# Kernel tuning notes

Hardware: AMD Instinct MI355X
Metric: run time of the kernel (lower is better)

Reference implementation:

```python
import jax, jax.numpy as jnp
import numpy as np

S, M, V, E, H = 128, 256, 32000, 1024, 512
PAD_ID = V - 1  # pad_id=-1 normalized to vocab-1


def setup_inputs() -> dict:
    key = jax.random.key(0)
    ks = jax.random.split(key, 9)
    F_lens = jax.random.randint(ks[0], (M,), 1, S + 1)
    tok = jax.random.randint(ks[1], (S, M), 1, PAD_ID)  # avoid 0 and PAD for valid tokens
    valid = jnp.arange(S)[:, None] < F_lens[None, :]
    F = jnp.where(valid, tok, PAD_ID)
    sc = 1.0 / np.sqrt(H)
    emb = jax.random.normal(ks[2], (V, E), jnp.float32) * 0.02
    emb = emb.at[PAD_ID].set(0.0)
    # PyTorch LSTM layout: gates [i, f, g, o]; bias_ih + bias_hh folded into one b.
    Wih0 = jax.random.uniform(ks[3], (2, 4 * H, E), jnp.float32, -sc, sc)
    Whh0 = jax.random.uniform(ks[4], (2, 4 * H, H), jnp.float32, -sc, sc)
    b0 = jax.random.uniform(ks[5], (2, 4 * H), jnp.float32, -sc, sc)
    Wih1 = jax.random.uniform(ks[6], (2, 4 * H, 2 * H), jnp.float32, -sc, sc)
    Whh1 = jax.random.uniform(ks[7], (2, 4 * H, H), jnp.float32, -sc, sc)
    b1 = jax.random.uniform(ks[8], (2, 4 * H), jnp.float32, -sc, sc)
    return dict(F=F, F_lens=F_lens, emb=emb, Wih0=Wih0, Whh0=Whh0, b0=b0,
                Wih1=Wih1, Whh1=Whh1, b1=b1)


def _run_lstm(x, mask, Wih, Whh, b):
    # x: [S, M, D], mask: [S, M] bool (update state only where valid, as packed seq does)
    m_ = x.shape[1]
    h_dim = Whh.shape[1]

    def step(carry, inp):
        h, c = carry
        xt, mt = inp
        g = xt @ Wih.T + h @ Whh.T + b
        i, f, gg, o = jnp.split(g, 4, axis=-1)
        c2 = jax.nn.sigmoid(f) * c + jax.nn.sigmoid(i) * jnp.tanh(gg)
        h2 = jax.nn.sigmoid(o) * jnp.tanh(c2)
        mt = mt[:, None]
        h2 = jnp.where(mt, h2, h)
        c2 = jnp.where(mt, c2, c)
        return (h2, c2), h2

    init = (jnp.zeros((m_, h_dim), x.dtype), jnp.zeros((m_, h_dim), x.dtype))
    _, hs = jax.lax.scan(step, init, (x, mask))
    return hs


def _bilstm_layer(x, mask, idx, Wih, Whh, b):
    # forward direction
    hf = _run_lstm(x, mask, Wih[0], Whh[0], b[0])
    # backward direction: per-sequence reverse within valid length (packed semantics)
    xr = jnp.take_along_axis(x, idx[:, :, None], axis=0)
    hb = _run_lstm(xr, mask, Wih[1], Whh[1], b[1])
    hb = jnp.take_along_axis(hb, idx[:, :, None], axis=0)  # idx is an involution on valid t
    return jnp.concatenate([hf, hb], axis=-1)


def reference(F, F_lens, emb, Wih0, Whh0, b0, Wih1, Whh1, b1):
    s_ = F.shape[0]
    t = jnp.arange(s_)[:, None]
    valid = t < F_lens[None, :]                      # [S, M]
    idx = jnp.where(valid, F_lens[None, :] - 1 - t, t)
    # embedding with padding_idx zeroing (matches nn.Embedding padding_idx + explicit loop)
    x = jnp.where((F != PAD_ID)[:, :, None], emb[F], 0.0)
    h1 = _bilstm_layer(x, valid, idx, Wih0, Whh0, b0)
    h2 = _bilstm_layer(h1, valid, idx, Wih1, Whh1, b1)
    # pad_packed_sequence(padding_value=h_pad=0) + final F==0 masking loop, fused
    keep = valid & (F != 0)
    return jnp.where(keep[:, :, None], h2, 0.0)
```

## Files before the change

kernel.cpp:

```cpp
#include <hip/hip_runtime.h>
#include <hip/hip_bf16.h>

#define S_LEN 128
#define M_B   256
#define E_DIM 1024
#define H_DIM 512
#define G4    2048
#define N_ROWS (S_LEN*M_B)
#define KD    1024

typedef __bf16 bf16_t;
typedef __bf16 bf16x8 __attribute__((ext_vector_type(8)));
typedef float  f32x4  __attribute__((ext_vector_type(4)));
typedef int    i32x4  __attribute__((ext_vector_type(4)));

#define AS1(p) ((const __attribute__((address_space(1))) void*)(p))
#define AS3(p) ((__attribute__((address_space(3))) void*)(p))

__device__ __forceinline__ float sigm(float x)     { return 1.f / (1.f + __expf(-x)); }
__device__ __forceinline__ float tanhfast(float x) { return 2.f / (1.f + __expf(-2.f * x)) - 1.f; }

__device__ __forceinline__ void store_h_dev(bf16_t* p, bf16_t v) {
    unsigned int w = (unsigned int)__builtin_bit_cast(unsigned short, v);
    asm volatile("global_store_short %0, %1, off sc0 sc1" :: "v"(p), "v"(w) : "memory");
}
__device__ __forceinline__ bf16x8 load_h_dev(const bf16_t* p) {
    i32x4 r;
    asm volatile("global_load_dwordx4 %0, %1, off sc0 sc1" : "=v"(r) : "v"(p) : "memory");
    return __builtin_bit_cast(bf16x8, r);
}
__device__ __forceinline__ float load_f32_async(const float* p) {
    float r;
    asm volatile("global_load_dword %0, %1, off" : "=v"(r) : "v"(p) : "memory");
    return r;
}

__global__ __launch_bounds__(256)
void permute_all_kernel(const float* __restrict__ Wih0, const float* __restrict__ Whh0,
                        const float* __restrict__ b0,
                        const float* __restrict__ Wih1, const float* __restrict__ Whh1,
                        const float* __restrict__ b1,
                        bf16_t* __restrict__ Wih0p, bf16_t* __restrict__ Whh0p,
                        bf16_t* __restrict__ Wih1p, bf16_t* __restrict__ Whh1p,
                        float* __restrict__ b0p, float* __restrict__ b1p)
{
    int bid = blockIdx.x;
    int lay = bid >> 12;
    int d   = (bid >> 11) & 1;
    int jp  = bid & 2047;
    int q = jp >> 6, r = jp & 63;
    int gate = r >> 4, u16 = r & 15;
    int j = gate * H_DIM + q * 16 + u16;

    const float* Wih = lay ? Wih1 : Wih0;
    const float* Whh = lay ? Whh1 : Whh0;
    const float* b   = lay ? b1 : b0;
    bf16_t* Wihp = lay ? Wih1p : Wih0p;
    bf16_t* Whhp = lay ? Whh1p : Whh0p;
    float*  bp   = lay ? b1p : b0p;

    const float* s_ih = Wih + ((size_t)d * G4 + j) * E_DIM;
    bf16_t*      d_ih = Wihp + ((size_t)d * G4 + jp) * E_DIM;
    for (int e = threadIdx.x; e < E_DIM; e += 256) d_ih[e] = (bf16_t)s_ih[e];

    const float* s_hh = Whh + ((size_t)d * G4 + j) * H_DIM;
    bf16_t*      d_hh = Whhp + ((size_t)d * G4 + jp) * H_DIM;
    for (int k = threadIdx.x; k < H_DIM; k += 256) d_hh[k] = (bf16_t)s_hh[k];

    if (threadIdx.x == 0) bp[d * G4 + jp] = b[d * G4 + j];
}

__global__ __launch_bounds__(256)
void embed_kernel(const int* __restrict__ F, const float* __restrict__ emb,
                  const int* __restrict__ F_lens,
                  bf16_t* __restrict__ X, int* __restrict__ srcrow)
{
    int n   = blockIdx.x;
    int tok = F[n];
    const float4* src = (const float4*)(emb + (size_t)tok * E_DIM);
    bf16_t*       dst = X + (size_t)n * E_DIM;
    for (int i = threadIdx.x; i < E_DIM / 4; i += 256) {
        float4 v = src[i];
        dst[i * 4 + 0] = (bf16_t)v.x;
        dst[i * 4 + 1] = (bf16_t)v.y;
        dst[i * 4 + 2] = (bf16_t)v.z;
        dst[i * 4 + 3] = (bf16_t)v.w;
    }
    if (threadIdx.x == 0) {
        int t = n >> 8, m = n & 255;
        int L = F_lens[m];
        int st = (t < L) ? (L - 1 - t) : t;
        srcrow[n] = st * M_B + m;
    }
}

#define BM 128
#define BN 128
#define BKG 64

__global__ __launch_bounds__(256)
void gemm_pre_kernel(const bf16_t* __restrict__ A,
                     const bf16_t* __restrict__ Wp,
                     const float* __restrict__ bp,
                     const int* __restrict__ srcrow,
                     float* __restrict__ PREc,
                     int rowbase, int TCR)
{
    const int nwg = gridDim.x;
    const int qx  = nwg >> 3;
    const int orig = blockIdx.x;
    const int wg   = (orig & 7) * qx + (orig >> 3);
    const int MT   = TCR / BM;
    const int n_t  = wg & 15;
    const int m_t  = (wg >> 4) % MT;
    const int d    = wg / (16 * MT);

    const int n0   = n_t * BN;
    const int mloc = m_t * BM;
    const int tid  = threadIdx.x;
    const int lane = tid & 63, wave = tid >> 6;
    const int wm = wave >> 1, wn = wave & 1;
    const int fr = lane & 15, fq = lane >> 4;

    __shared__ __attribute__((aligned(16))) bf16_t At[BM * BKG];
    __shared__ __attribute__((aligned(16))) bf16_t Bt[BN * BKG];

    const int rA = tid >> 3;
    const int co = (((tid & 7) ^ (rA & 7)) << 3);
    size_t srowA[4];
    const bf16_t* Bp[4];
#pragma unroll
    for (int it = 0; it < 4; ++it) {
        int nn = rowbase + mloc + rA + it * 32;
        srowA[it] = (d == 1) ? (size_t)srcrow[nn] : (size_t)nn;
        Bp[it] = Wp + ((size_t)d * G4 + n0 + rA + it * 32) * KD + co;
    }

    f32x4 acc[4][4];
#pragma unroll
    for (int i = 0; i < 4; ++i)
#pragma unroll
        for (int j = 0; j < 4; ++j) { f32x4 z = {0.f, 0.f, 0.f, 0.f}; acc[i][j] = z; }

    for (int kt = 0; kt < KD; kt += BKG) {
#pragma unroll
        for (int it = 0; it < 4; ++it)
            __builtin_amdgcn_global_load_lds(AS1(A + srowA[it] * KD + kt + co),
                                             AS3(&At[(it * 256 + wave * 64) * 8]), 16, 0, 0);
#pragma unroll
        for (int it = 0; it < 4; ++it)
            __builtin_amdgcn_global_load_lds(AS1(Bp[it] + kt),
                                             AS3(&Bt[(it * 256 + wave * 64) * 8]), 16, 0, 0);
        __syncthreads();

        bf16x8 af[2][4], bff[2][4];
#pragma unroll
        for (int ks = 0; ks < 2; ++ks) {
#pragma unroll
            for (int i = 0; i < 4; ++i) {
                int ra = wm * 64 + i * 16 + fr;
                int ca = (ks * 4 + fq) ^ (ra & 7);
                af[ks][i] = *(const bf16x8*)&At[ra * BKG + ca * 8];
                int rb = wn * 64 + i * 16 + fr;
                int cbk = (ks * 4 + fq) ^ (rb & 7);
                bff[ks][i] = *(const bf16x8*)&Bt[rb * BKG + cbk * 8];
            }
        }
#pragma unroll
        for (int ks = 0; ks < 2; ++ks)
#pragma unroll
            for (int i = 0; i < 4; ++i)
#pragma unroll
                for (int j = 0; j < 4; ++j)
                    acc[i][j] = __builtin_amdgcn_mfma_f32_16x16x32_bf16(af[ks][i], bff[ks][j], acc[i][j], 0, 0, 0);
        __syncthreads();
    }

    const int cb = n0 + wn * 64 + fr;
#pragma unroll
    for (int mi = 0; mi < 4; ++mi) {
#pragma unroll
        for (int rr = 0; rr < 4; ++rr) {
            int r = mloc + wm * 64 + mi * 16 + fq * 4 + rr;
            float* prow = PREc + ((size_t)d * TCR + r) * G4;
#pragma unroll
            for (int ni = 0; ni < 4; ++ni) {
                int col = cb + ni * 16;
                prow[col] = acc[mi][ni][rr] + bp[d * G4 + col];
            }
        }
    }
}

__global__ __launch_bounds__(256)
void lstm_chunk_kernel(const bf16_t* __restrict__ Whhp,
                       const float* __restrict__ PREc,
                       const int* __restrict__ F_lens,
                       float* __restrict__ cfb,
                       bf16_t* __restrict__ hbA,
                       bf16_t* __restrict__ hbB,
                       bf16_t* __restrict__ H1,
                       float* __restrict__ OUT,
                       unsigned int* __restrict__ ctr,
                       int t0, int TC, int TCR, int mode, int s_base)
{
    const int d  = blockIdx.z;
    const int bx = blockIdx.x;
    const int m0 = blockIdx.y * 64;
    const int tid = threadIdx.x;
    const int lane = tid & 63, wave = tid >> 6;
    const int fr = lane & 15, fq = lane >> 4;
    const int gslot = ((blockIdx.y << 1) | d) * 16;

    __shared__ __attribute__((aligned(16))) bf16_t Bt[64 * 512];

    const bf16_t* Bg = Whhp + ((size_t)d * G4 + bx * 64) * H_DIM;
#pragma unroll
    for (int it = 0; it < 16; ++it) {
        int c   = it * 256 + tid;
        int row = c >> 6, ck = c & 63;
        int cks = ck ^ (row & 7);
        __builtin_amdgcn_global_load_lds(AS1(Bg + (size_t)row * H_DIM + cks * 8),
                                         AS3(&Bt[(it * 256 + wave * 64) * 8]), 16, 0, 0);
    }

    const int mrow  = m0 + wave * 16 + fr;
    const int u     = bx * 16 + fr;
    const int cbcol = bx * 64 + fr;
    int mm[4], LL[4], sidx[4];
    float c_own[4], h_own[4];
    const float* pbase[4];
#pragma unroll
    for (int rr = 0; rr < 4; ++rr) {
        mm[rr]   = m0 + wave * 16 + fq * 4 + rr;
        LL[rr]   = F_lens[mm[rr]];
        sidx[rr] = (d * M_B + mm[rr]) * H_DIM + u;
        c_own[rr]= cfb[sidx[rr]];
        pbase[rr]= PREc + ((size_t)d * TCR + mm[rr]) * G4 + cbcol;
    }
    {
        const bf16_t* hin0 = (t0 & 1) ? hbB : hbA;
#pragma unroll
        for (int rr = 0; rr < 4; ++rr) h_own[rr] = (float)hin0[sidx[rr]];
    }

    float pv[4][4];
#pragma unroll
    for (int rr = 0; rr < 4; ++rr) {
#pragma unroll
        for (int g = 0; g < 4; ++g)
            pv[rr][g] = load_f32_async(pbase[rr] + g * 16);
    }

    __syncthreads();

    for (int tt = 0; tt < TC; ++tt) {
        const int t = t0 + tt;
        const bf16_t* hin  = (t & 1) ? hbB : hbA;
        bf16_t*       hout = (t & 1) ? hbA : hbB;

        const bf16_t* Arow = hin + ((size_t)d * M_B + mrow) * H_DIM + fq * 8;
        bf16x8 af[16];
#pragma unroll
        for (int ks = 0; ks < 16; ++ks)
            af[ks] = load_h_dev(Arow + ks * 32);
        asm volatile("s_waitcnt vmcnt(0)" ::: "memory");
        __builtin_amdgcn_sched_barrier(0);

        f32x4 acc[4];
#pragma unroll
        for (int j = 0; j < 4; ++j) { f32x4 z = {0.f, 0.f, 0.f, 0.f}; acc[j] = z; }

#pragma unroll
        for (int ks = 0; ks < 16; ++ks) {
#pragma unroll
            for (int j = 0; j < 4; ++j) {
                int rb = j * 16 + fr;
                int ck = (ks * 4 + fq) ^ (rb & 7);
                bf16x8 bf = *(const bf16x8*)&Bt[rb * 512 + ck * 8];
                acc[j] = __builtin_amdgcn_mfma_f32_16x16x32_bf16(af[ks], bf, acc[j], 0, 0, 0);
            }
        }

#pragma unroll
        for (int rr = 0; rr < 4; ++rr) {
            bool mt = (t < LL[rr]);
            float gi = acc[0][rr] + pv[rr][0];
            float gf = acc[1][rr] + pv[rr][1];
            float gg = acc[2][rr] + pv[rr][2];
            float go = acc[3][rr] + pv[rr][3];
            float c2 = sigm(gf) * c_own[rr] + sigm(gi) * tanhfast(gg);
            float h2 = sigm(go) * tanhfast(c2);
            if (!mt) { c2 = c_own[rr]; h2 = h_own[rr]; }
            c_own[rr] = c2;
            h_own[rr] = h2;
            store_h_dev(&hout[sidx[rr]], (bf16_t)h2);
        }
        asm volatile("s_waitcnt vmcnt(0)" ::: "memory");
        __syncthreads();
        if (tid == 0)
            __hip_atomic_fetch_add(&ctr[gslot], 1u, __ATOMIC_RELAXED, __HIP_MEMORY_SCOPE_AGENT);

#pragma unroll
        for (int rr = 0; rr < 4; ++rr) {
            bool mt = (t < LL[rr]);
            int trow = (d == 0 || !mt) ? t : (LL[rr] - 1 - t);
            size_t orow = (size_t)trow * M_B + mm[rr];
            if (mode == 0) H1[orow * 1024 + d * H_DIM + u] = (bf16_t)h_own[rr];
            else           OUT[orow * 1024 + d * H_DIM + u] = mt ? h_own[rr] : 0.f;
        }
        float pvn[4][4];
        if (tt + 1 < TC) {
#pragma unroll
            for (int rr = 0; rr < 4; ++rr) {
                const float* prow = pbase[rr] + (size_t)(tt + 1) * ((size_t)M_B * G4);
#pragma unroll
                for (int g = 0; g < 4; ++g)
                    pvn[rr][g] = load_f32_async(prow + g * 16);
            }
        }

        if (tid == 0) {
            unsigned int tgt = (unsigned int)(s_base + tt + 1) * 32u;
            while (__hip_atomic_load(&ctr[gslot], __ATOMIC_RELAXED, __HIP_MEMORY_SCOPE_AGENT) < tgt)
                __builtin_amdgcn_s_sleep(2);
        }
        __syncthreads();

        if (tt + 1 < TC) {
#pragma unroll
            for (int rr = 0; rr < 4; ++rr)
#pragma unroll
                for (int g = 0; g < 4; ++g)
                    pv[rr][g] = pvn[rr][g];
        }
    }

#pragma unroll
    for (int rr = 0; rr < 4; ++rr) cfb[sidx[rr]] = c_own[rr];
}

extern "C" void kernel_launch(void* const* d_in, const int* in_sizes, int n_in,
                              void* d_out, int out_size, void* d_ws, size_t ws_size,
                              hipStream_t stream)
{
    const int*   F      = (const int*)d_in[0];
    const int*   F_lens = (const int*)d_in[1];
    const float* emb    = (const float*)d_in[2];
    const float* Wih0   = (const float*)d_in[3];
    const float* Whh0   = (const float*)d_in[4];
    const float* b0     = (const float*)d_in[5];
    const float* Wih1   = (const float*)d_in[6];
    const float* Whh1   = (const float*)d_in[7];
    const float* b1     = (const float*)d_in[8];
    float* OUT = (float*)d_out;

    char* p = (char*)d_ws;
    auto alloc = [&](size_t bytes) { char* q = p; p += (bytes + 255) & ~(size_t)255; return (void*)q; };
    bf16_t* X0    = (bf16_t*)alloc((size_t)N_ROWS * E_DIM * 2);
    bf16_t* H1    = (bf16_t*)alloc((size_t)N_ROWS * 1024 * 2);
    bf16_t* Wih0p = (bf16_t*)alloc((size_t)2 * G4 * E_DIM * 2);
    bf16_t* Whh0p = (bf16_t*)alloc((size_t)2 * G4 * H_DIM * 2);
    bf16_t* Wih1p = (bf16_t*)alloc((size_t)2 * G4 * E_DIM * 2);
    bf16_t* Whh1p = (bf16_t*)alloc((size_t)2 * G4 * H_DIM * 2);
    float*  b0p   = (float*)alloc((size_t)2 * G4 * 4);
    float*  b1p   = (float*)alloc((size_t)2 * G4 * 4);
    int*    srcrow= (int*)alloc((size_t)N_ROWS * 4);
    bf16_t* hbA   = (bf16_t*)alloc((size_t)2 * M_B * H_DIM * 2);
    bf16_t* hbB   = (bf16_t*)alloc((size_t)2 * M_B * H_DIM * 2);
    float*  cfb   = (float*)alloc((size_t)2 * M_B * H_DIM * 4);
    unsigned int* ctr = (unsigned int*)alloc(512);
    size_t base_used = (size_t)(p - (char*)d_ws);

    int TC = 0;
    const int tcs[6] = {32, 16, 8, 4, 2, 1};
    for (int i = 0; i < 6; ++i) {
        size_t need = base_used + (size_t)2 * tcs[i] * M_B * G4 * 4;
        if (need <= ws_size) { TC = tcs[i]; break; }
    }
    if (TC == 0) return;
    float* PREc = (float*)p;
    const int TCR = TC * M_B;

    hipMemsetAsync(ctr, 0, 512, stream);
    permute_all_kernel<<<dim3(2 * 2 * G4), 256, 0, stream>>>(
        Wih0, Whh0, b0, Wih1, Whh1, b1, Wih0p, Whh0p, Wih1p, Whh1p, b0p, b1p);
    embed_kernel<<<dim3(N_ROWS), 256, 0, stream>>>(F, emb, F_lens, X0, srcrow);

    for (int layer = 0; layer < 2; ++layer) {
        const bf16_t* Xin  = layer ? H1 : X0;
        const bf16_t* Wihp = layer ? Wih1p : Wih0p;
        const bf16_t* Whhp = layer ? Whh1p : Whh0p;
        const float*  bp   = layer ? b1p : b0p;

        hipMemsetAsync(hbA, 0, (size_t)2 * M_B * H_DIM * 2, stream);
        hipMemsetAsync(cfb, 0, (size_t)2 * M_B * H_DIM * 4, stream);

        for (int c = 0; c < S_LEN / TC; ++c) {
            gemm_pre_kernel<<<dim3(2 * (TCR / BM) * 16), 256, 0, stream>>>(
                Xin, Wihp, bp, srcrow, PREc, c * TCR, TCR);

            lstm_chunk_kernel<<<dim3(32, 4, 2), dim3(256), 0, stream>>>(
                Whhp, PREc, F_lens, cfb, hbA, hbB, H1, OUT, ctr,
                c * TC, TC, TCR, layer, layer * S_LEN + c * TC);
        }
    }
}
```

Before: 2.418 ms.

## Fuse input projection into persistent LSTM layer kernel, drop precomputed gate buffer

Measured after the change: 5.757 ms. 138% more time.

```diff
diff --git a/kernel.cpp b/kernel.cpp
--- a/kernel.cpp
+++ b/kernel.cpp
@@ -7,7 +7,6 @@
 #define H_DIM 512
 #define G4    2048
 #define N_ROWS (S_LEN*M_B)
-#define KD    1024
 
 typedef __bf16 bf16_t;
 typedef __bf16 bf16x8 __attribute__((ext_vector_type(8)));
@@ -28,11 +27,6 @@
     i32x4 r;
     asm volatile("global_load_dwordx4 %0, %1, off sc0 sc1" : "=v"(r) : "v"(p) : "memory");
     return __builtin_bit_cast(bf16x8, r);
-}
-__device__ __forceinline__ float load_f32_async(const float* p) {
-    float r;
-    asm volatile("global_load_dword %0, %1, off" : "=v"(r) : "v"(p) : "memory");
-    return r;
 }
 
 __global__ __launch_bounds__(256)
@@ -72,8 +66,7 @@
 
 __global__ __launch_bounds__(256)
 void embed_kernel(const int* __restrict__ F, const float* __restrict__ emb,
-                  const int* __restrict__ F_lens,
-                  bf16_t* __restrict__ X, int* __restrict__ srcrow)
+                  bf16_t* __restrict__ X)
 {
     int n   = blockIdx.x;
     int tok = F[n];
@@ -86,124 +79,22 @@
         dst[i * 4 + 2] = (bf16_t)v.z;
         dst[i * 4 + 3] = (bf16_t)v.w;
     }
-    if (threadIdx.x == 0) {
-        int t = n >> 8, m = n & 255;
-        int L = F_lens[m];
-        int st = (t < L) ? (L - 1 - t) : t;
-        srcrow[n] = st * M_B + m;
-    }
-}
-
-#define BM 128
-#define BN 128
-#define BKG 64
+}
 
 __global__ __launch_bounds__(256)
-void gemm_pre_kernel(const bf16_t* __restrict__ A,
-                     const bf16_t* __restrict__ Wp,
-                     const float* __restrict__ bp,
-                     const int* __restrict__ srcrow,
-                     float* __restrict__ PREc,
-                     int rowbase, int TCR)
-{
-    const int nwg = gridDim.x;
-    const int qx  = nwg >> 3;
-    const int orig = blockIdx.x;
-    const int wg   = (orig & 7) * qx + (orig >> 3);
-    const int MT   = TCR / BM;
-    const int n_t  = wg & 15;
-    const int m_t  = (wg >> 4) % MT;
-    const int d    = wg / (16 * MT);
-
-    const int n0   = n_t * BN;
-    const int mloc = m_t * BM;
-    const int tid  = threadIdx.x;
-    const int lane = tid & 63, wave = tid >> 6;
-    const int wm = wave >> 1, wn = wave & 1;
-    const int fr = lane & 15, fq = lane >> 4;
-
-    __shared__ __attribute__((aligned(16))) bf16_t At[BM * BKG];
-    __shared__ __attribute__((aligned(16))) bf16_t Bt[BN * BKG];
-
-    const int rA = tid >> 3;
-    const int co = (((tid & 7) ^ (rA & 7)) << 3);
-    size_t srowA[4];
-    const bf16_t* Bp[4];
-#pragma unroll
-    for (int it = 0; it < 4; ++it) {
-        int nn = rowbase + mloc + rA + it * 32;
-        srowA[it] = (d == 1) ? (size_t)srcrow[nn] : (size_t)nn;
-        Bp[it] = Wp + ((size_t)d * G4 + n0 + rA + it * 32) * KD + co;
-    }
-
-    f32x4 acc[4][4];
-#pragma unroll
-    for (int i = 0; i < 4; ++i)
-#pragma unroll
-        for (int j = 0; j < 4; ++j) { f32x4 z = {0.f, 0.f, 0.f, 0.f}; acc[i][j] = z; }
-
-    for (int kt = 0; kt < KD; kt += BKG) {
-#pragma unroll
-        for (int it = 0; it < 4; ++it)
-            __builtin_amdgcn_global_load_lds(AS1(A + srowA[it] * KD + kt + co),
-                                             AS3(&At[(it * 256 + wave * 64) * 8]), 16, 0, 0);
-#pragma unroll
-        for (int it = 0; it < 4; ++it)
-            __builtin_amdgcn_global_load_lds(AS1(Bp[it] + kt),
-                                             AS3(&Bt[(it * 256 + wave * 64) * 8]), 16, 0, 0);
-        __syncthreads();
-
-        bf16x8 af[2][4], bff[2][4];
-#pragma unroll
-        for (int ks = 0; ks < 2; ++ks) {
-#pragma unroll
-            for (int i = 0; i < 4; ++i) {
-                int ra = wm * 64 + i * 16 + fr;
-                int ca = (ks * 4 + fq) ^ (ra & 7);
-                af[ks][i] = *(const bf16x8*)&At[ra * BKG + ca * 8];
-                int rb = wn * 64 + i * 16 + fr;
-                int cbk = (ks * 4 + fq) ^ (rb & 7);
-                bff[ks][i] = *(const bf16x8*)&Bt[rb * BKG + cbk * 8];
-            }
-        }
-#pragma unroll
-        for (int ks = 0; ks < 2; ++ks)
-#pragma unroll
-            for (int i = 0; i < 4; ++i)
-#pragma unroll
-                for (int j = 0; j < 4; ++j)
-                    acc[i][j] = __builtin_amdgcn_mfma_f32_16x16x32_bf16(af[ks][i], bff[ks][j], acc[i][j], 0, 0, 0);
-        __syncthreads();
-    }
-
-    const int cb = n0 + wn * 64 + fr;
-#pragma unroll
-    for (int mi = 0; mi < 4; ++mi) {
-#pragma unroll
-        for (int rr = 0; rr < 4; ++rr) {
-            int r = mloc + wm * 64 + mi * 16 + fq * 4 + rr;
-            float* prow = PREc + ((size_t)d * TCR + r) * G4;
-#pragma unroll
-            for (int ni = 0; ni < 4; ++ni) {
-                int col = cb + ni * 16;
-                prow[col] = acc[mi][ni][rr] + bp[d * G4 + col];
-            }
-        }
-    }
-}
-
-__global__ __launch_bounds__(256)
-void lstm_chunk_kernel(const bf16_t* __restrict__ Whhp,
-                       const float* __restrict__ PREc,
+void lstm_layer_kernel(const bf16_t* __restrict__ Whhp,
+                       const bf16_t* __restrict__ Wihp,
+                       const float* __restrict__ bp,
+                       const bf16_t* __restrict__ Xin,
                        const int* __restrict__ F_lens,
-                       float* __restrict__ cfb,
                        bf16_t* __restrict__ hbA,
                        bf16_t* __restrict__ hbB,
                        bf16_t* __restrict__ H1,
                        float* __restrict__ OUT,
                        unsigned int* __restrict__ ctr,
-                       int t0, int TC, int TCR, int mode, int s_base)
-{
+                       int mode, int s_base)
+{
+    const int TC = S_LEN;
     const int d  = blockIdx.z;
     const int bx = blockIdx.x;
     const int m0 = blockIdx.y * 64;
@@ -227,68 +118,83 @@
     const int mrow  = m0 + wave * 16 + fr;
     const int u     = bx * 16 + fr;
     const int cbcol = bx * 64 + fr;
+    const int Lm    = F_lens[mrow];
     int mm[4], LL[4], sidx[4];
     float c_own[4], h_own[4];
-    const float* pbase[4];
+    float bias[4];
+    const bf16_t* wihb[4];
+#pragma unroll
+    for (int j = 0; j < 4; ++j) {
+        bias[j] = bp[d * G4 + cbcol + j * 16];
+        wihb[j] = Wihp + ((size_t)d * G4 + bx * 64 + j * 16 + fr) * E_DIM + fq * 8;
+    }
 #pragma unroll
     for (int rr = 0; rr < 4; ++rr) {
         mm[rr]   = m0 + wave * 16 + fq * 4 + rr;
         LL[rr]   = F_lens[mm[rr]];
         sidx[rr] = (d * M_B + mm[rr]) * H_DIM + u;
-        c_own[rr]= cfb[sidx[rr]];
-        pbase[rr]= PREc + ((size_t)d * TCR + mm[rr]) * G4 + cbcol;
-    }
+        c_own[rr] = 0.f;
+        h_own[rr] = 0.f;
+    }
+
+    f32x4 acc[4];
+#pragma unroll
+    for (int j = 0; j < 4; ++j) { f32x4 z = {0.f, 0.f, 0.f, 0.f}; acc[j] = z; }
     {
-        const bf16_t* hin0 = (t0 & 1) ? hbB : hbA;
-#pragma unroll
-        for (int rr = 0; rr < 4; ++rr) h_own[rr] = (float)hin0[sidx[rr]];
-    }
-
-    float pv[4][4];
-#pragma unroll
-    for (int rr = 0; rr < 4; ++rr) {
-#pragma unroll
-        for (int g = 0; g < 4; ++g)
-            pv[rr][g] = load_f32_async(pbase[rr] + g * 16);
+        const int trx = (d == 0) ? 0 : (Lm - 1);
+        const bf16_t* Xrow = Xin + ((size_t)trx * M_B + mrow) * E_DIM + fq * 8;
+#pragma unroll
+        for (int half = 0; half < 2; ++half) {
+            bf16x8 ax[16];
+#pragma unroll
+            for (int ks = 0; ks < 16; ++ks)
+                ax[ks] = *(const bf16x8*)(Xrow + half * 512 + ks * 32);
+#pragma unroll
+            for (int ks = 0; ks < 16; ++ks) {
+#pragma unroll
+                for (int j = 0; j < 4; ++j) {
+                    bf16x8 bw = *(const bf16x8*)(wihb[j] + half * 512 + ks * 32);
+                    acc[j] = __builtin_amdgcn_mfma_f32_16x16x32_bf16(ax[ks], bw, acc[j], 0, 0, 0);
+                }
+            }
+        }
     }
 
     __syncthreads();
 
     for (int tt = 0; tt < TC; ++tt) {
-        const int t = t0 + tt;
+        const int t = tt;
         const bf16_t* hin  = (t & 1) ? hbB : hbA;
         bf16_t*       hout = (t & 1) ? hbA : hbB;
 
-        const bf16_t* Arow = hin + ((size_t)d * M_B + mrow) * H_DIM + fq * 8;
-        bf16x8 af[16];
-#pragma unroll
-        for (int ks = 0; ks < 16; ++ks)
-            af[ks] = load_h_dev(Arow + ks * 32);
-        asm volatile("s_waitcnt vmcnt(0)" ::: "memory");
-        __builtin_amdgcn_sched_barrier(0);
-
-        f32x4 acc[4];
-#pragma unroll
-        for (int j = 0; j < 4; ++j) { f32x4 z = {0.f, 0.f, 0.f, 0.f}; acc[j] = z; }
-
-#pragma unroll
-        for (int ks = 0; ks < 16; ++ks) {
-#pragma unroll
-            for (int j = 0; j < 4; ++j) {
-                int rb = j * 16 + fr;
-                int ck = (ks * 4 + fq) ^ (rb & 7);
-                bf16x8 bf = *(const bf16x8*)&Bt[rb * 512 + ck * 8];
-                acc[j] = __builtin_amdgcn_mfma_f32_16x16x32_bf16(af[ks], bf, acc[j], 0, 0, 0);
+        if (t > 0) {
+            const bf16_t* Arow = hin + ((size_t)d * M_B + mrow) * H_DIM + fq * 8;
+            bf16x8 af[16];
+#pragma unroll
+            for (int ks = 0; ks < 16; ++ks)
+                af[ks] = load_h_dev(Arow + ks * 32);
+            asm volatile("s_waitcnt vmcnt(0)" ::: "memory");
+            __builtin_amdgcn_sched_barrier(0);
+
+#pragma unroll
+            for (int ks = 0; ks < 16; ++ks) {
+#pragma unroll
+                for (int j = 0; j < 4; ++j) {
+                    int rb = j * 16 + fr;
+                    int ck = (ks * 4 + fq) ^ (rb & 7);
+                    bf16x8 bf = *(const bf16x8*)&Bt[rb * 512 + ck * 8];
+                    acc[j] = __builtin_amdgcn_mfma_f32_16x16x32_bf16(af[ks], bf, acc[j], 0, 0, 0);
+                }
             }
         }
 
 #pragma unroll
         for (int rr = 0; rr < 4; ++rr) {
             bool mt = (t < LL[rr]);
-            float gi = acc[0][rr] + pv[rr][0];
-            float gf = acc[1][rr] + pv[rr][1];
-            float gg = acc[2][rr] + pv[rr][2];
-            float go = acc[3][rr] + pv[rr][3];
+            float gi = acc[0][rr] + bias[0];
+            float gf = acc[1][rr] + bias[1];
+            float gg = acc[2][rr] + bias[2];
+            float go = acc[3][rr] + bias[3];
             float c2 = sigm(gf) * c_own[rr] + sigm(gi) * tanhfast(gg);
             float h2 = sigm(go) * tanhfast(c2);
             if (!mt) { c2 = c_own[rr]; h2 = h_own[rr]; }
@@ -309,14 +215,27 @@
             if (mode == 0) H1[orow * 1024 + d * H_DIM + u] = (bf16_t)h_own[rr];
             else           OUT[orow * 1024 + d * H_DIM + u] = mt ? h_own[rr] : 0.f;
         }
-        float pvn[4][4];
+
+#pragma unroll
+        for (int j = 0; j < 4; ++j) { f32x4 z = {0.f, 0.f, 0.f, 0.f}; acc[j] = z; }
         if (tt + 1 < TC) {
-#pragma unroll
-            for (int rr = 0; rr < 4; ++rr) {
-                const float* prow = pbase[rr] + (size_t)(tt + 1) * ((size_t)M_B * G4);
-#pragma unroll
-                for (int g = 0; g < 4; ++g)
-                    pvn[rr][g] = load_f32_async(prow + g * 16);
+            const int tn  = t + 1;
+            const int trx = (d == 0 || tn >= Lm) ? tn : (Lm - 1 - tn);
+            const bf16_t* Xrow = Xin + ((size_t)trx * M_B + mrow) * E_DIM + fq * 8;
+#pragma unroll
+            for (int half = 0; half < 2; ++half) {
+                bf16x8 ax[16];
+#pragma unroll
+                for (int ks = 0; ks < 16; ++ks)
+                    ax[ks] = *(const bf16x8*)(Xrow + half * 512 + ks * 32);
+#pragma unroll
+                for (int ks = 0; ks < 16; ++ks) {
+#pragma unroll
+                    for (int j = 0; j < 4; ++j) {
+                        bf16x8 bw = *(const bf16x8*)(wihb[j] + half * 512 + ks * 32);
+                        acc[j] = __builtin_amdgcn_mfma_f32_16x16x32_bf16(ax[ks], bw, acc[j], 0, 0, 0);
+                    }
+                }
             }
         }
 
@@ -326,18 +245,7 @@
                 __builtin_amdgcn_s_sleep(2);
         }
         __syncthreads();
-
-        if (tt + 1 < TC) {
-#pragma unroll
-            for (int rr = 0; rr < 4; ++rr)
-#pragma unroll
-                for (int g = 0; g < 4; ++g)
-                    pv[rr][g] = pvn[rr][g];
-        }
-    }
-
-#pragma unroll
-    for (int rr = 0; rr < 4; ++rr) cfb[sidx[rr]] = c_own[rr];
+    }
 }
 
 extern "C" void kernel_launch(void* const* d_in, const int* in_sizes, int n_in,
@@ -365,44 +273,18 @@
     bf16_t* Whh1p = (bf16_t*)alloc((size_t)2 * G4 * H_DIM * 2);
     float*  b0p   = (float*)alloc((size_t)2 * G4 * 4);
     float*  b1p   = (float*)alloc((size_t)2 * G4 * 4);
-    int*    srcrow= (int*)alloc((size_t)N_ROWS * 4);
     bf16_t* hbA   = (bf16_t*)alloc((size_t)2 * M_B * H_DIM * 2);
     bf16_t* hbB   = (bf16_t*)alloc((size_t)2 * M_B * H_DIM * 2);
-    float*  cfb   = (float*)alloc((size_t)2 * M_B * H_DIM * 4);
     unsigned int* ctr = (unsigned int*)alloc(512);
-    size_t base_used = (size_t)(p - (char*)d_ws);
-
-    int TC = 0;
-    const int tcs[6] = {32, 16, 8, 4, 2, 1};
-    for (int i = 0; i < 6; ++i) {
-        size_t need = base_used + (size_t)2 * tcs[i] * M_B * G4 * 4;
-        if (need <= ws_size) { TC = tcs[i]; break; }
-    }
-    if (TC == 0) return;
-    float* PREc = (float*)p;
-    const int TCR = TC * M_B;
+    if (ws_size < (size_t)(p - (char*)d_ws)) return;
 
     hipMemsetAsync(ctr, 0, 512, stream);
     permute_all_kernel<<<dim3(2 * 2 * G4), 256, 0, stream>>>(
         Wih0, Whh0, b0, Wih1, Whh1, b1, Wih0p, Whh0p, Wih1p, Whh1p, b0p, b1p);
-    embed_kernel<<<dim3(N_ROWS), 256, 0, stream>>>(F, emb, F_lens, X0, srcrow);
-
-    for (int layer = 0; layer < 2; ++layer) {
-        const bf16_t* Xin  = layer ? H1 : X0;
-        const bf16_t* Wihp = layer ? Wih1p : Wih0p;
-        const bf16_t* Whhp = layer ? Whh1p : Whh0p;
-        const float*  bp   = layer ? b1p : b0p;
-
-        hipMemsetAsync(hbA, 0, (size_t)2 * M_B * H_DIM * 2, stream);
-        hipMemsetAsync(cfb, 0, (size_t)2 * M_B * H_DIM * 4, stream);
-
-        for (int c = 0; c < S_LEN / TC; ++c) {
-            gemm_pre_kernel<<<dim3(2 * (TCR / BM) * 16), 256, 0, stream>>>(
-                Xin, Wihp, bp, srcrow, PREc, c * TCR, TCR);
-
-            lstm_chunk_kernel<<<dim3(32, 4, 2), dim3(256), 0, stream>>>(
-                Whhp, PREc, F_lens, cfb, hbA, hbB, H1, OUT, ctr,
-                c * TC, TC, TCR, layer, layer * S_LEN + c * TC);
-        }
-    }
-}
+    embed_kernel<<<dim3(N_ROWS), 256, 0, stream>>>(F, emb, X0);
+
+    lstm_layer_kernel<<<dim3(32, 4, 2), dim3(256), 0, stream>>>(
+        Whh0p, Wih0p, b0p, X0, F_lens, hbA, hbB, H1, OUT, ctr, 0, 0);
+    lstm_layer_kernel<<<dim3(32, 4, 2), dim3(256), 0, stream>>>(
+        Whh1p, Wih1p, b1p, H1, F_lens, hbA, hbB, H1, OUT, ctr, 1, S_LEN);
+}
```
